# Kernel optimization log

Hardware: AMD Instinct MI355X
Metric: run time of the kernel (lower is better)

## Reference

```python
import jax, jax.numpy as jnp
import numpy as np

D_MODEL = 1024
NUM_HEADS = 16
HEAD_DIM = D_MODEL // NUM_HEADS
WINDOW = 16
DILATION = 3
SCALE = HEAD_DIM ** -0.5


def _linear(x, W, b):
    # torch nn.Linear: y = x @ W.T + b, W: [out, in]
    return x @ W.T + b


def _chunk_attention(x, Wq, bq, Wk, bk, Wv, bv, chunk):
    B, L, D = x.shape
    pad = (-L) % chunk
    if pad:
        x = jnp.pad(x, ((0, 0), (0, pad), (0, 0)))
    Lp = L + pad
    nC = Lp // chunk
    xr = x.reshape(B * nC, chunk, D)  # [BC, c, D]

    def heads(t):
        return t.reshape(B * nC, chunk, NUM_HEADS, HEAD_DIM).transpose(0, 2, 1, 3)

    q = heads(_linear(xr, Wq, bq))  # [BC, H, c, hd]
    k = heads(_linear(xr, Wk, bk))
    v = heads(_linear(xr, Wv, bv))
    attn = jax.nn.softmax(jnp.einsum('bhqd,bhkd->bhqk', q, k) * SCALE, axis=-1)
    out = jnp.einsum('bhqk,bhkd->bhqd', attn, v)  # [BC, H, c, hd]
    out = out.transpose(0, 2, 1, 3).reshape(B, Lp, D)
    return out[:, :L, :]


def setup_inputs() -> dict:
    key = jax.random.key(0)
    ks = jax.random.split(key, 9)
    s = 1.0 / np.sqrt(D_MODEL)
    x = jax.random.normal(ks[0], (4, 4096, D_MODEL), dtype=jnp.float32)
    def lin(kw, kb):
        W = jax.random.uniform(kw, (D_MODEL, D_MODEL), minval=-s, maxval=s, dtype=jnp.float32)
        b = jax.random.uniform(kb, (D_MODEL,), minval=-s, maxval=s, dtype=jnp.float32)
        return W, b
    Wq, bq = lin(ks[1], ks[2])
    Wk, bk = lin(ks[3], ks[4])
    Wv, bv = lin(ks[5], ks[6])
    Wo, bo = lin(ks[7], ks[8])
    return {"x": x, "Wq": Wq, "bq": bq, "Wk": Wk, "bk": bk,
            "Wv": Wv, "bv": bv, "Wo": Wo, "bo": bo}


def reference(x, Wq, bq, Wk, bk, Wv, bv, Wo, bo):
    B, L, D = x.shape
    # local windowed attention
    local_out = _chunk_attention(x, Wq, bq, Wk, bk, Wv, bv, WINDOW)
    # dilated (atrous) attention: stride-DILATION interleave via reshape/permute
    pad = (-L) % DILATION
    x_pad = jnp.pad(x, ((0, 0), (0, pad), (0, 0))) if pad else x
    Lp = L + pad
    xv = x_pad.reshape(B, Lp // DILATION, DILATION, D).transpose(0, 2, 1, 3)
    x_atrous = xv.reshape(B * DILATION, Lp // DILATION, D)
    a = _chunk_attention(x_atrous, Wq, bq, Wk, bk, Wv, bv, WINDOW)
    a = a.reshape(B, DILATION, Lp // DILATION, D).transpose(0, 2, 1, 3).reshape(B, Lp, D)
    atrous_out = a[:, :L, :]
    return _linear(local_out + atrous_out, Wo, bo)
```

## Files before the change

kernel.cpp:

```cpp
#include <hip/hip_runtime.h>
#include <hip/hip_bf16.h>
#include <stdint.h>

typedef unsigned short ushort_t;
typedef __attribute__((ext_vector_type(8))) short bf16x8;
typedef __attribute__((ext_vector_type(4))) float f32x4;

__device__ __forceinline__ ushort_t f2bf(float f) {
    uint32_t u = __builtin_bit_cast(uint32_t, f);
    u += 0x7FFF + ((u >> 16) & 1);
    return (ushort_t)(u >> 16);
}
__device__ __forceinline__ float bf2f(ushort_t h) {
    return __builtin_bit_cast(float, (uint32_t)h << 16);
}

__device__ __forceinline__ f32x4 mfma16(bf16x8 a, bf16x8 b, f32x4 c) {
    return __builtin_amdgcn_mfma_f32_16x16x32_bf16(a, b, c, 0, 0, 0);
}

#define GLL(g, l) __builtin_amdgcn_global_load_lds(                              \
    (const __attribute__((address_space(1))) void*)(g),                          \
    (__attribute__((address_space(3))) void*)(l), 16, 0, 0)

#define CFENCE asm volatile("" ::: "memory")
#define BARRIER do { CFENCE; __builtin_amdgcn_s_barrier(); CFENCE; } while (0)
#define PRIO1 __builtin_amdgcn_s_setprio(1)
#define PRIO0 __builtin_amdgcn_s_setprio(0)
#define PH_SYNC do { BARRIER;                                                    \
    asm volatile("s_waitcnt lgkmcnt(0)" ::: "memory"); } while (0)


__device__ __forceinline__ void cvt8(const float* s, ushort_t* d) {
    float4 a = ((const float4*)s)[0], b = ((const float4*)s)[1];
    union { bf16x8 v; ushort_t u[8]; } o;
    o.u[0] = f2bf(a.x); o.u[1] = f2bf(a.y); o.u[2] = f2bf(a.z); o.u[3] = f2bf(a.w);
    o.u[4] = f2bf(b.x); o.u[5] = f2bf(b.y); o.u[6] = f2bf(b.z); o.u[7] = f2bf(b.w);
    *(bf16x8*)d = o.v;
}

__global__ __launch_bounds__(256) void cvt_all(
    const float* __restrict__ x,
    const float* __restrict__ Wq, const float* __restrict__ Wk,
    const float* __restrict__ Wv, const float* __restrict__ Wo,
    const float* __restrict__ bq, const float* __restrict__ bk,
    const float* __restrict__ bv,
    ushort_t* __restrict__ xb, ushort_t* __restrict__ wqkv,
    float* __restrict__ bqkv)
{
    const int NX = 16384 * 1024 / 8;
    const int NW = 1024 * 1024 / 8;
    int i = blockIdx.x * 256 + threadIdx.x;
    if (i < NX) {
        cvt8(x + (size_t)i * 8, xb + (size_t)i * 8);
    } else if (i < NX + 4 * NW) {
        int j = i - NX;
        int w = j >> 17, off = j & (NW - 1);
        const float* s = (w == 0) ? Wq : (w == 1) ? Wk : (w == 2) ? Wv : Wo;
        cvt8(s + (size_t)off * 8, wqkv + (size_t)j * 8);
    } else if (i < NX + 4 * NW + 384) {
        int j = i - NX - 4 * NW;
        int w2 = j >> 7, off = j & 127;
        const float* s = (w2 == 0) ? bq : (w2 == 1) ? bk : bv;
        ((float4*)(bqkv + j * 8))[0] = ((const float4*)(s + off * 8))[0];
        ((float4*)(bqkv + j * 8))[1] = ((const float4*)(s + off * 8))[1];
    }
}


#define STG(P, rb, slot, h, kt) {                                                \
    _Pragma("unroll")                                                            \
    for (int j = 0; j < 2; ++j) {                                                \
        int idx = j * 512 + tid; int row = idx >> 3, ch = idx & 7;               \
        GLL(P + (size_t)((rb) + (h) * 128 + row) * 1024 + (kt) * 64              \
              + ((ch ^ (row & 7)) * 8),                                          \
            (char*)(slot) + (size_t)idx * 16);                                   \
    } }

#define LDA4(d, mibase)                                                          \
    _Pragma("unroll")                                                            \
    for (int q = 0; q < 4; ++q)                                                  \
        _Pragma("unroll")                                                        \
        for (int kk = 0; kk < 2; ++kk)                                           \
            a[q][kk] = *(const bf16x8*)&As[(d) * 2 + wm]                         \
                [((mibase) + q) * 1024 + ln * 64 + cho[kk]];

#define LDB2(d, nibase)                                                          \
    _Pragma("unroll")                                                            \
    for (int q = 0; q < 2; ++q)                                                  \
        _Pragma("unroll")                                                        \
        for (int kk = 0; kk < 2; ++kk)                                           \
            bfr[(nibase) + q][kk] = *(const bf16x8*)&Bs[(d) * 2 + bh]            \
                [brow0 + ((nibase) + q) * 1024 + ln * 64 + cho[kk]];

#define MFMA_Q(qm, qn)                                                           \
    _Pragma("unroll")                                                            \
    for (int mi = 0; mi < 4; ++mi)                                               \
        _Pragma("unroll")                                                        \
        for (int nl = 0; nl < 2; ++nl) {                                         \
            acc[(qm)*4+mi][(qn)*2+nl] =                                          \
                mfma16(a[mi][0], bfr[(qn)*2+nl][0], acc[(qm)*4+mi][(qn)*2+nl]);  \
            acc[(qm)*4+mi][(qn)*2+nl] =                                          \
                mfma16(a[mi][1], bfr[(qn)*2+nl][1], acc[(qm)*4+mi][(qn)*2+nl]);  \
        }

template<int MODE>
__global__ __launch_bounds__(512, 2) void gemm8(
    const ushort_t* __restrict__ A, const ushort_t* __restrict__ B,
    const float* __restrict__ bias, void* __restrict__ outp,
    int M, int NTN)
{
    __shared__ ushort_t As[4][128 * 64];
    __shared__ ushort_t Bs[4][128 * 64];

    const int bid = blockIdx.x;
    const int nwg = gridDim.x;
    const int q8 = nwg >> 3;
    const int swz = (bid & 7) * q8 + (bid >> 3);
    const int m0 = (swz / NTN) * 256;
    const int n0 = (swz % NTN) * 256;

    const int tid = threadIdx.x;
    const int wave = tid >> 6, lane = tid & 63;
    const int wm = wave >> 2, wn = wave & 3;
    const int lg = lane >> 4, ln = lane & 15;
    const int bh = wn >> 1;
    const int brow0 = (wn & 1) * 4096;
    int cho[2];
    cho[0] = ((0 * 4 + lg) ^ (ln & 7)) * 8;
    cho[1] = ((1 * 4 + lg) ^ (ln & 7)) * 8;

    f32x4 acc[8][4];
#pragma unroll
    for (int i2 = 0; i2 < 8; ++i2)
#pragma unroll
        for (int j2 = 0; j2 < 4; ++j2) acc[i2][j2] = (f32x4){0.f, 0.f, 0.f, 0.f};

    STG(A, m0, &As[0][0], 0, 0)
    STG(A, m0, &As[1][0], 1, 0)
    STG(B, n0, &Bs[0][0], 0, 0)
    STG(B, n0, &Bs[1][0], 1, 0)
    STG(B, n0, &Bs[2][0], 0, 1)
    STG(B, n0, &Bs[3][0], 1, 1)
    asm volatile("s_waitcnt vmcnt(4)" ::: "memory");
    BARRIER;

    for (int i = 0; i < 8; ++i) {
        const int kA1 = 2 * i + 1;
        const int kN  = 2 * i + 2;
        const int kN1 = 2 * i + 3;
        const bool pf = (i < 7);
        bf16x8 a[4][2], bfr[4][2];

        LDA4(0, 0) LDB2(0, 0)
        STG(A, m0, &As[2][0], 0, kA1)
        PH_SYNC; PRIO1; MFMA_Q(0, 0) PRIO0;
        BARRIER;
        LDB2(0, 2)
        STG(A, m0, &As[3][0], 1, kA1)
        PH_SYNC; PRIO1; MFMA_Q(0, 1) PRIO0;
        BARRIER;
        LDA4(0, 4)
        if (pf) STG(B, n0, &Bs[0][0], 0, kN)
        PH_SYNC; PRIO1; MFMA_Q(1, 0) PRIO0;
        BARRIER;
        if (pf) STG(B, n0, &Bs[1][0], 1, kN)
        PRIO1; MFMA_Q(1, 1) PRIO0;
        if (pf) { asm volatile("s_waitcnt vmcnt(4)" ::: "memory"); }
        else    { asm volatile("s_waitcnt vmcnt(0)" ::: "memory"); }
        BARRIER;
        LDA4(1, 0) LDB2(1, 0)
        if (pf) STG(A, m0, &As[0][0], 0, kN)
        PH_SYNC; PRIO1; MFMA_Q(0, 0) PRIO0;
        BARRIER;
        LDB2(1, 2)
        if (pf) STG(A, m0, &As[1][0], 1, kN)
        PH_SYNC; PRIO1; MFMA_Q(0, 1) PRIO0;
        BARRIER;
        LDA4(1, 4)
        if (pf) STG(B, n0, &Bs[2][0], 0, kN1)
        PH_SYNC; PRIO1; MFMA_Q(1, 0) PRIO0;
        BARRIER;
        if (pf) STG(B, n0, &Bs[3][0], 1, kN1)
        PRIO1; MFMA_Q(1, 1) PRIO0;
        if (pf) { asm volatile("s_waitcnt vmcnt(4)" ::: "memory"); }
        else    { asm volatile("s_waitcnt vmcnt(0)" ::: "memory"); }
        BARRIER;
    }

    float bval[4];
#pragma unroll
    for (int ni = 0; ni < 4; ++ni) bval[ni] = bias[n0 + wn * 64 + ni * 16 + ln];

    if (MODE == 0) {
        ushort_t* obase = (ushort_t*)outp + (size_t)(n0 >> 10) * ((size_t)M * 1024)
                          + (n0 & 1023) + wn * 64 + ln;
#pragma unroll
        for (int mi = 0; mi < 8; ++mi) {
#pragma unroll
            for (int r = 0; r < 4; ++r) {
                int m = m0 + wm * 128 + mi * 16 + lg * 4 + r;
                ushort_t* orow = obase + (size_t)m * 1024;
#pragma unroll
                for (int ni = 0; ni < 4; ++ni)
                    orow[ni * 16] = f2bf(acc[mi][ni][r] + bval[ni]);
            }
        }
    } else {
        float* obase = (float*)outp + n0 + wn * 64 + ln;
#pragma unroll
        for (int mi = 0; mi < 8; ++mi) {
#pragma unroll
            for (int r = 0; r < 4; ++r) {
                int m = m0 + wm * 128 + mi * 16 + lg * 4 + r;
                float* orow = obase + (size_t)m * 1024;
#pragma unroll
                for (int ni = 0; ni < 4; ++ni)
                    orow[ni * 16] = acc[mi][ni][r] + bval[ni];
            }
        }
    }
}


__device__ __forceinline__ bf16x8 bias8(const float* __restrict__ b, int off) {
    float4 f0 = *(const float4*)(b + off);
    float4 f1 = *(const float4*)(b + off + 4);
    union { bf16x8 v; ushort_t u[8]; } o;
    o.u[0] = f2bf(f0.x); o.u[1] = f2bf(f0.y); o.u[2] = f2bf(f0.z); o.u[3] = f2bf(f0.w);
    o.u[4] = f2bf(f1.x); o.u[5] = f2bf(f1.y); o.u[6] = f2bf(f1.z); o.u[7] = f2bf(f1.w);
    return o.v;
}


__global__ __launch_bounds__(256) void attn_local(
    const ushort_t* __restrict__ Q, const ushort_t* __restrict__ K,
    const ushort_t* __restrict__ V, ushort_t* __restrict__ S)
{
    const int wave = threadIdx.x >> 6, lane = threadIdx.x & 63;
    const int unit = blockIdx.x * 4 + wave;
    const int h = unit & 15;
    const int c = unit >> 4;
    const int g = lane >> 4, nn = lane & 15;
    __shared__ ushort_t lds_p[4][16 * 16];
    __shared__ ushort_t vt[4][64 * 16];

    const size_t rowb = (size_t)c * 16;
    size_t aoff = (rowb + nn) * 1024 + h * 64 + g * 8;
    bf16x8 qa0 = *(const bf16x8*)(Q + aoff);
    bf16x8 qa1 = *(const bf16x8*)(Q + aoff + 32);
    bf16x8 kb0 = *(const bf16x8*)(K + aoff);
    bf16x8 kb1 = *(const bf16x8*)(K + aoff + 32);

#pragma unroll
    for (int it = 0; it < 2; ++it) {
        int u = it * 64 + lane;
        int n = u >> 3, cc = u & 7;
        bf16x8 vv = *(const bf16x8*)(V + (rowb + n) * 1024 + h * 64 + cc * 8);
        union { bf16x8 v; ushort_t u8[8]; } vu; vu.v = vv;
#pragma unroll
        for (int j = 0; j < 8; ++j) vt[wave][(cc * 8 + j) * 16 + n] = vu.u8[j];
    }

    f32x4 sc = {0.f, 0.f, 0.f, 0.f};
    sc = mfma16(qa0, kb0, sc);
    sc = mfma16(qa1, kb1, sc);

#pragma unroll
    for (int r = 0; r < 4; ++r) {
        float s = sc[r] * 0.125f;
        float mx = s;
#pragma unroll
        for (int off = 1; off < 16; off <<= 1) mx = fmaxf(mx, __shfl_xor(mx, off, 64));
        float e = __expf(s - mx);
        float sm = e;
#pragma unroll
        for (int off = 1; off < 16; off <<= 1) sm += __shfl_xor(sm, off, 64);
        lds_p[wave][(g * 4 + r) * 16 + nn] = f2bf(e / sm);
    }
    CFENCE;

    bf16x8 zero8 = {};
    bf16x8 pa = (g < 2) ? *(const bf16x8*)&lds_p[wave][nn * 16 + g * 8] : zero8;
#pragma unroll
    for (int dt = 0; dt < 4; ++dt) {
        bf16x8 vb = (g < 2) ? *(const bf16x8*)&vt[wave][(dt * 16 + nn) * 16 + g * 8] : zero8;
        f32x4 o = mfma16(pa, vb, (f32x4){0.f, 0.f, 0.f, 0.f});
#pragma unroll
        for (int r = 0; r < 4; ++r) {
            size_t orow = rowb + g * 4 + r;
            S[orow * 1024 + h * 64 + dt * 16 + nn] = f2bf(o[r]);
        }
    }
}


__global__ __launch_bounds__(256) void attn_atrous(
    const ushort_t* __restrict__ Q, const ushort_t* __restrict__ K,
    const ushort_t* __restrict__ V,
    const float* __restrict__ bq, const float* __restrict__ bk,
    const float* __restrict__ bv, ushort_t* __restrict__ S)
{
    const int wave = threadIdx.x >> 6, lane = threadIdx.x & 63;
    const int unit = blockIdx.x * 4 + wave;
    const int h = unit & 15;
    const int tmp = unit >> 4;
    const int c = tmp % 86;
    const int sidx = tmp / 86;
    const int b = sidx / 3, dil = sidx % 3;
    const int g = lane >> 4, nn = lane & 15;
    __shared__ ushort_t lds_p[4][16 * 16];
    __shared__ ushort_t vt[4][64 * 16];

    const int dof = h * 64 + g * 8;
    const int p_n = 3 * (c * 16 + nn) + dil;
    bf16x8 qa0, qa1, kb0, kb1;
    if (p_n < 4096) {
        size_t o = ((size_t)b * 4096 + p_n) * 1024 + dof;
        qa0 = *(const bf16x8*)(Q + o);
        qa1 = *(const bf16x8*)(Q + o + 32);
        kb0 = *(const bf16x8*)(K + o);
        kb1 = *(const bf16x8*)(K + o + 32);
    } else {
        qa0 = bias8(bq, dof); qa1 = bias8(bq, dof + 32);
        kb0 = bias8(bk, dof); kb1 = bias8(bk, dof + 32);
    }

#pragma unroll
    for (int it = 0; it < 2; ++it) {
        int u = it * 64 + lane;
        int n = u >> 3, cc = u & 7;
        int p_v = 3 * (c * 16 + n) + dil;
        bf16x8 vv = (p_v < 4096)
            ? *(const bf16x8*)(V + ((size_t)b * 4096 + p_v) * 1024 + h * 64 + cc * 8)
            : bias8(bv, h * 64 + cc * 8);
        union { bf16x8 v; ushort_t u8[8]; } vu; vu.v = vv;
#pragma unroll
        for (int j = 0; j < 8; ++j) vt[wave][(cc * 8 + j) * 16 + n] = vu.u8[j];
    }

    f32x4 sc = {0.f, 0.f, 0.f, 0.f};
    sc = mfma16(qa0, kb0, sc);
    sc = mfma16(qa1, kb1, sc);

#pragma unroll
    for (int r = 0; r < 4; ++r) {
        float s = sc[r] * 0.125f;
        float mx = s;
#pragma unroll
        for (int off = 1; off < 16; off <<= 1) mx = fmaxf(mx, __shfl_xor(mx, off, 64));
        float e = __expf(s - mx);
        float sm = e;
#pragma unroll
        for (int off = 1; off < 16; off <<= 1) sm += __shfl_xor(sm, off, 64);
        lds_p[wave][(g * 4 + r) * 16 + nn] = f2bf(e / sm);
    }
    CFENCE;

    bf16x8 zero8 = {};
    bf16x8 pa = (g < 2) ? *(const bf16x8*)&lds_p[wave][nn * 16 + g * 8] : zero8;
#pragma unroll
    for (int dt = 0; dt < 4; ++dt) {
        bf16x8 vb = (g < 2) ? *(const bf16x8*)&vt[wave][(dt * 16 + nn) * 16 + g * 8] : zero8;
        f32x4 o = mfma16(pa, vb, (f32x4){0.f, 0.f, 0.f, 0.f});
#pragma unroll
        for (int r = 0; r < 4; ++r) {
            int p_q = 3 * (c * 16 + g * 4 + r) + dil;
            if (p_q < 4096) {
                size_t off = ((size_t)b * 4096 + p_q) * 1024 + h * 64 + dt * 16 + nn;
                S[off] = f2bf(bf2f(S[off]) + o[r]);
            }
        }
    }
}


extern "C" void kernel_launch(void* const* d_in, const int* in_sizes, int n_in,
                              void* d_out, int out_size, void* d_ws, size_t ws_size,
                              hipStream_t stream)
{
    const float* x  = (const float*)d_in[0];
    const float* Wq = (const float*)d_in[1];
    const float* bq = (const float*)d_in[2];
    const float* Wk = (const float*)d_in[3];
    const float* bk = (const float*)d_in[4];
    const float* Wv = (const float*)d_in[5];
    const float* bv = (const float*)d_in[6];
    const float* Wo = (const float*)d_in[7];
    const float* bo = (const float*)d_in[8];
    float* out = (float*)d_out;

    const size_t NT = 16384;
    ushort_t* xb   = (ushort_t*)d_ws;
    ushort_t* wqkv = xb + NT * 1024;
    ushort_t* wo   = wqkv + 3 * 1024 * 1024;
    ushort_t* Qb   = wo + 1024 * 1024;
    ushort_t* Kb   = Qb + NT * 1024;
    ushort_t* Vb   = Kb + NT * 1024;
    ushort_t* Sb   = Vb + NT * 1024;
    float*    bqkv = (float*)(Sb + NT * 1024);

    const int total_units = 2097152 + 4 * 131072 + 384;
    cvt_all<<<(total_units + 255) / 256, 256, 0, stream>>>(
        x, Wq, Wk, Wv, Wo, bq, bk, bv, xb, wqkv, bqkv);

    gemm8<0><<<768, 512, 0, stream>>>(xb, wqkv, bqkv, (void*)Qb, (int)NT, 12);

    attn_local <<<4096, 256, 0, stream>>>(Qb, Kb, Vb, Sb);
    attn_atrous<<<4128, 256, 0, stream>>>(Qb, Kb, Vb, bq, bk, bv, Sb);

    gemm8<1><<<256, 512, 0, stream>>>(Sb, wo, bo, (void*)out, (int)NT, 4);
}
```

Measured before the change: 348.9 us.

## Restructure GEMM mainloop to K=32 slices with 4-stage ring and fewer barriers

The bf16 GEMM mainloop now stages 256x32 K-slices of A and B into a four-buffer LDS ring, keeping three slices in flight instead of the previous 128x64 half-tiles. LDS fragment reads for the next phase are issued before the current MFMA block, and the per-phase barrier plus lgkmcnt wait is replaced by one barrier per K-slice. The goal is to cut synchronization overhead and hide LDS and global latency behind MFMAs. In exchange there are twice as many K iterations with smaller loads, and it relies on the compiler inserting correct LDS waits on its own.

Result: no change. 344.9 us (-1.1%).

```diff
diff --git a/kernel.cpp b/kernel.cpp
--- a/kernel.cpp
+++ b/kernel.cpp
@@ -27,8 +27,8 @@
 #define BARRIER do { CFENCE; __builtin_amdgcn_s_barrier(); CFENCE; } while (0)
 #define PRIO1 __builtin_amdgcn_s_setprio(1)
 #define PRIO0 __builtin_amdgcn_s_setprio(0)
-#define PH_SYNC do { BARRIER;                                                    \
-    asm volatile("s_waitcnt lgkmcnt(0)" ::: "memory"); } while (0)
+#define VM4 asm volatile("s_waitcnt vmcnt(4)" ::: "memory")
+#define VM0 asm volatile("s_waitcnt vmcnt(0)" ::: "memory")
 
 
 __device__ __forceinline__ void cvt8(const float* s, ushort_t* d) {
@@ -68,50 +68,42 @@
 }
 
 
-#define STG(P, rb, slot, h, kt) {                                                \
-    _Pragma("unroll")                                                            \
+#define STGA(bq, kt) { _Pragma("unroll")                                         \
     for (int j = 0; j < 2; ++j) {                                                \
-        int idx = j * 512 + tid; int row = idx >> 3, ch = idx & 7;               \
-        GLL(P + (size_t)((rb) + (h) * 128 + row) * 1024 + (kt) * 64              \
-              + ((ch ^ (row & 7)) * 8),                                          \
-            (char*)(slot) + (size_t)idx * 16);                                   \
+        int idx = j * 512 + tid; int row = idx >> 2, ch = idx & 3;               \
+        GLL(A + (size_t)(m0 + row) * 1024 + (kt) * 32 + ((ch ^ (row & 3)) * 8),  \
+            (char*)&As[bq][0] + (size_t)idx * 16);                               \
     } }
-
-#define LDA4(d, mibase)                                                          \
-    _Pragma("unroll")                                                            \
+#define STGB(bq, kt) { _Pragma("unroll")                                         \
+    for (int j = 0; j < 2; ++j) {                                                \
+        int idx = j * 512 + tid; int row = idx >> 2, ch = idx & 3;               \
+        GLL(B + (size_t)(n0 + row) * 1024 + (kt) * 32 + ((ch ^ (row & 3)) * 8),  \
+            (char*)&Bs[bq][0] + (size_t)idx * 16);                               \
+    } }
+
+#define RD4(dst, bq, mibase) { _Pragma("unroll")                                 \
     for (int q = 0; q < 4; ++q)                                                  \
-        _Pragma("unroll")                                                        \
-        for (int kk = 0; kk < 2; ++kk)                                           \
-            a[q][kk] = *(const bf16x8*)&As[(d) * 2 + wm]                         \
-                [((mibase) + q) * 1024 + ln * 64 + cho[kk]];
-
-#define LDB2(d, nibase)                                                          \
-    _Pragma("unroll")                                                            \
-    for (int q = 0; q < 2; ++q)                                                  \
-        _Pragma("unroll")                                                        \
-        for (int kk = 0; kk < 2; ++kk)                                           \
-            bfr[(nibase) + q][kk] = *(const bf16x8*)&Bs[(d) * 2 + bh]            \
-                [brow0 + ((nibase) + q) * 1024 + ln * 64 + cho[kk]];
-
-#define MFMA_Q(qm, qn)                                                           \
-    _Pragma("unroll")                                                            \
-    for (int mi = 0; mi < 4; ++mi)                                               \
-        _Pragma("unroll")                                                        \
-        for (int nl = 0; nl < 2; ++nl) {                                         \
-            acc[(qm)*4+mi][(qn)*2+nl] =                                          \
-                mfma16(a[mi][0], bfr[(qn)*2+nl][0], acc[(qm)*4+mi][(qn)*2+nl]);  \
-            acc[(qm)*4+mi][(qn)*2+nl] =                                          \
-                mfma16(a[mi][1], bfr[(qn)*2+nl][1], acc[(qm)*4+mi][(qn)*2+nl]);  \
-        }
+        dst[q] = *(const bf16x8*)&As[bq][(wm * 128 + ((mibase) + q) * 16 + ln)   \
+                                        * 32 + cho]; }
+#define RDB(dst, bq) { _Pragma("unroll")                                         \
+    for (int q = 0; q < 4; ++q)                                                  \
+        dst[q] = *(const bf16x8*)&Bs[bq][(wn * 64 + q * 16 + ln) * 32 + cho]; }
+
+#define MFMA16(mibase, av, bv) { _Pragma("unroll")                               \
+    for (int mi = 0; mi < 4; ++mi) _Pragma("unroll")                             \
+        for (int ni = 0; ni < 4; ++ni)                                           \
+            acc[(mibase) + mi][ni] =                                             \
+                mfma16(av[mi], bv[ni], acc[(mibase) + mi][ni]); }
 
 template<int MODE>
-__global__ __launch_bounds__(512, 2) void gemm8(
+__global__ __launch_bounds__(512, 2) void gemm6(
     const ushort_t* __restrict__ A, const ushort_t* __restrict__ B,
     const float* __restrict__ bias, void* __restrict__ outp,
     int M, int NTN)
 {
-    __shared__ ushort_t As[4][128 * 64];
-    __shared__ ushort_t Bs[4][128 * 64];
+    __shared__ ushort_t As[4][256 * 32];
+    __shared__ ushort_t Bs[4][256 * 32];
+    const int NK = 32;
 
     const int bid = blockIdx.x;
     const int nwg = gridDim.x;
@@ -124,11 +116,7 @@
     const int wave = tid >> 6, lane = tid & 63;
     const int wm = wave >> 2, wn = wave & 3;
     const int lg = lane >> 4, ln = lane & 15;
-    const int bh = wn >> 1;
-    const int brow0 = (wn & 1) * 4096;
-    int cho[2];
-    cho[0] = ((0 * 4 + lg) ^ (ln & 7)) * 8;
-    cho[1] = ((1 * 4 + lg) ^ (ln & 7)) * 8;
+    const int cho = (lg ^ (ln & 3)) * 8;
 
     f32x4 acc[8][4];
 #pragma unroll
@@ -136,55 +124,40 @@
 #pragma unroll
         for (int j2 = 0; j2 < 4; ++j2) acc[i2][j2] = (f32x4){0.f, 0.f, 0.f, 0.f};
 
-    STG(A, m0, &As[0][0], 0, 0)
-    STG(A, m0, &As[1][0], 1, 0)
-    STG(B, n0, &Bs[0][0], 0, 0)
-    STG(B, n0, &Bs[1][0], 1, 0)
-    STG(B, n0, &Bs[2][0], 0, 1)
-    STG(B, n0, &Bs[3][0], 1, 1)
-    asm volatile("s_waitcnt vmcnt(4)" ::: "memory");
+    STGA(0, 0) STGB(0, 0)
+    STGA(1, 1) STGB(1, 1)
+    STGA(2, 2) STGB(2, 2)
+    VM4;
     BARRIER;
 
-    for (int i = 0; i < 8; ++i) {
-        const int kA1 = 2 * i + 1;
-        const int kN  = 2 * i + 2;
-        const int kN1 = 2 * i + 3;
-        const bool pf = (i < 7);
-        bf16x8 a[4][2], bfr[4][2];
-
-        LDA4(0, 0) LDB2(0, 0)
-        STG(A, m0, &As[2][0], 0, kA1)
-        PH_SYNC; PRIO1; MFMA_Q(0, 0) PRIO0;
+    bf16x8 aE0[4], aE1[4], aO0[4], aO1[4], bE[4], bO[4];
+    RD4(aE0, 0, 0) RDB(bE, 0)
+
+    for (int it = 0; it < 16; ++it) {
+        const int ke = 2 * it, ko = ke + 1;
+        const int ce = (it & 1) << 1, co = ce | 1;
+        const int s1 = (ke + 3) & 3;
+        const int s2 = ce;
+        const bool p1 = (ke + 3 < NK), p2 = (ko + 3 < NK);
+
+        RD4(aE1, ce, 4)
+        if (p1) STGA(s1, ke + 3)
+        PRIO1; MFMA16(0, aE0, bE) PRIO0;
+
+        RD4(aO0, co, 0) RDB(bO, co)
+        if (p1) STGB(s1, ke + 3)
+        PRIO1; MFMA16(4, aE1, bE) PRIO0;
+        if (p1) { VM4; } else { VM0; }
         BARRIER;
-        LDB2(0, 2)
-        STG(A, m0, &As[3][0], 1, kA1)
-        PH_SYNC; PRIO1; MFMA_Q(0, 1) PRIO0;
-        BARRIER;
-        LDA4(0, 4)
-        if (pf) STG(B, n0, &Bs[0][0], 0, kN)
-        PH_SYNC; PRIO1; MFMA_Q(1, 0) PRIO0;
-        BARRIER;
-        if (pf) STG(B, n0, &Bs[1][0], 1, kN)
-        PRIO1; MFMA_Q(1, 1) PRIO0;
-        if (pf) { asm volatile("s_waitcnt vmcnt(4)" ::: "memory"); }
-        else    { asm volatile("s_waitcnt vmcnt(0)" ::: "memory"); }
-        BARRIER;
-        LDA4(1, 0) LDB2(1, 0)
-        if (pf) STG(A, m0, &As[0][0], 0, kN)
-        PH_SYNC; PRIO1; MFMA_Q(0, 0) PRIO0;
-        BARRIER;
-        LDB2(1, 2)
-        if (pf) STG(A, m0, &As[1][0], 1, kN)
-        PH_SYNC; PRIO1; MFMA_Q(0, 1) PRIO0;
-        BARRIER;
-        LDA4(1, 4)
-        if (pf) STG(B, n0, &Bs[2][0], 0, kN1)
-        PH_SYNC; PRIO1; MFMA_Q(1, 0) PRIO0;
-        BARRIER;
-        if (pf) STG(B, n0, &Bs[3][0], 1, kN1)
-        PRIO1; MFMA_Q(1, 1) PRIO0;
-        if (pf) { asm volatile("s_waitcnt vmcnt(4)" ::: "memory"); }
-        else    { asm volatile("s_waitcnt vmcnt(0)" ::: "memory"); }
+
+        RD4(aO1, co, 4)
+        if (p2) STGA(s2, ko + 3)
+        PRIO1; MFMA16(0, aO0, bO) PRIO0;
+
+        if (it + 1 < 16) { RD4(aE0, (ce + 2) & 3, 0) RDB(bE, (ce + 2) & 3) }
+        if (p2) STGB(s2, ko + 3)
+        PRIO1; MFMA16(4, aO1, bO) PRIO0;
+        if (p2) { VM4; } else { VM0; }
         BARRIER;
     }
 
@@ -404,10 +377,10 @@
     cvt_all<<<(total_units + 255) / 256, 256, 0, stream>>>(
         x, Wq, Wk, Wv, Wo, bq, bk, bv, xb, wqkv, bqkv);
 
-    gemm8<0><<<768, 512, 0, stream>>>(xb, wqkv, bqkv, (void*)Qb, (int)NT, 12);
+    gemm6<0><<<768, 512, 0, stream>>>(xb, wqkv, bqkv, (void*)Qb, (int)NT, 12);
 
     attn_local <<<4096, 256, 0, stream>>>(Qb, Kb, Vb, Sb);
     attn_atrous<<<4128, 256, 0, stream>>>(Qb, Kb, Vb, bq, bk, bv, Sb);
 
-    gemm8<1><<<256, 512, 0, stream>>>(Sb, wo, bo, (void*)out, (int)NT, 4);
-}
+    gemm6<1><<<256, 512, 0, stream>>>(Sb, wo, bo, (void*)out, (int)NT, 4);
+}
```
